# Performance work log

Hardware: AMD Instinct MI355X
Metric: run time of the kernel (lower is better)

Reference implementation:

```python
import jax, jax.numpy as jnp
import numpy as np

N_NODES = 100000
N_EDGES = 1600000
D_IN = 64
D_HID = 64
N_LAYERS = 3


def setup_inputs() -> dict:
    key = jax.random.key(0)
    ks = jax.random.split(key, 10)
    inp = {
        "node_feat": jax.random.normal(ks[0], (N_NODES, D_IN), dtype=jnp.float32),
        "src": jax.random.randint(ks[1], (N_EDGES,), 0, N_NODES, dtype=jnp.int32),
        "dst": jax.random.randint(ks[2], (N_EDGES,), 0, N_NODES, dtype=jnp.int32),
        "graph_len": jnp.ones((1,), dtype=jnp.int32) * N_NODES,
    }
    # GraphConv weights: shape (in_feats, out_feats), applied as feat @ W + b (DGL xavier-style init)
    dims = [D_IN] + [D_HID] * N_LAYERS
    for i in range(N_LAYERS):
        scale = float(np.sqrt(2.0 / (dims[i] + dims[i + 1])))
        inp[f"W{i}"] = jax.random.normal(ks[3 + i], (dims[i], dims[i + 1]), dtype=jnp.float32) * scale
        inp[f"b{i}"] = jnp.zeros((dims[i + 1],), dtype=jnp.float32)
    return inp


def reference(node_feat, src, dst, graph_len, W0, b0, W1, b1, W2, b2):
    n = node_feat.shape[0]
    e = src.shape[0]
    ones = jnp.ones((e,), dtype=node_feat.dtype)
    # DGL GraphConv norm='both': src-side out-degree^{-1/2}, dst-side in-degree^{-1/2}, clamp(min=1)
    deg_out = jax.ops.segment_sum(ones, src, num_segments=n)
    deg_in = jax.ops.segment_sum(ones, dst, num_segments=n)
    inv_sqrt_out = jax.lax.rsqrt(jnp.clip(deg_out, 1.0, None))[:, None]  # [N,1]
    inv_sqrt_in = jax.lax.rsqrt(jnp.clip(deg_in, 1.0, None))[:, None]    # [N,1]

    def graph_conv(x, W, b):
        msg = (x * inv_sqrt_out)[src]                              # [E,F] gather
        agg = jax.ops.segment_sum(msg, dst, num_segments=n)        # [N,F] scatter-add
        return (agg * inv_sqrt_in) @ W + b                         # SpMM result -> dense linear

    xs = []
    h = node_feat
    for W, b in ((W0, b0), (W1, b1), (W2, b2)):
        h = jax.nn.relu(graph_conv(h, W, b))
        xs.append(h)

    # Faithful to source: torch.sum(x, dim=1) -> per-node scalar [N]; concat over layers -> [3N]
    x_pool = jnp.concatenate([x.sum(axis=1) for x in xs], axis=-1)
    xs_cat = jnp.concatenate(xs, axis=-1)  # [N, 3*H]
    return x_pool, xs_cat
```

## Files before the change

kernel.cpp:

```cpp
#include <hip/hip_runtime.h>


#define TPB 256
#define CAP_S2 10240

__device__ __forceinline__ unsigned short f2bf(float f) {
  unsigned u = __float_as_uint(f);
  u += 0x7fff + ((u >> 16) & 1);
  return (unsigned short)(u >> 16);
}
__device__ __forceinline__ float bflo(unsigned u) { return __uint_as_float(u << 16); }
__device__ __forceinline__ float bfhi(unsigned u) { return __uint_as_float(u & 0xffff0000u); }

__global__ __launch_bounds__(256) void coarse_hist(
    const int* __restrict__ src, const int* __restrict__ dst, int e,
    int* __restrict__ bhS, int* __restrict__ bhD) {
  __shared__ int hs[256], hd[256];
  int t = threadIdx.x, b = blockIdx.x;
  hs[t] = 0; hd[t] = 0;
  __syncthreads();
  int base = b * 4096;
  #pragma unroll
  for (int k = 0; k < 4; k++) {
    int i = base + 4 * t + 1024 * k;
    if (i + 3 < e) {
      int4 s4 = *(const int4*)&src[i];
      int4 d4 = *(const int4*)&dst[i];
      atomicAdd(&hs[s4.x >> 9], 1); atomicAdd(&hs[s4.y >> 9], 1);
      atomicAdd(&hs[s4.z >> 9], 1); atomicAdd(&hs[s4.w >> 9], 1);
      atomicAdd(&hd[d4.x >> 9], 1); atomicAdd(&hd[d4.y >> 9], 1);
      atomicAdd(&hd[d4.z >> 9], 1); atomicAdd(&hd[d4.w >> 9], 1);
    } else {
      for (int j = i; j < e && j < i + 4; j++) {
        atomicAdd(&hs[src[j] >> 9], 1);
        atomicAdd(&hd[dst[j] >> 9], 1);
      }
    }
  }
  __syncthreads();
  bhS[b * 256 + t] = hs[t];
  bhD[b * 256 + t] = hd[t];
}

__global__ __launch_bounds__(256) void scan_blocks(
    int* __restrict__ bhS, int* __restrict__ bhD, int nblk, int nbb,
    int* __restrict__ c_base_s, int* __restrict__ c_base_d,
    int* __restrict__ row_ptr, int n, int e) {
  __shared__ int lds[256];
  int t = threadIdx.x;
  int* bh = (blockIdx.x == 0) ? bhS : bhD;
  int run = 0;
  int b = 0;
  for (; b + 3 < nblk; b += 4) {
    int i0 = (b + 0) * 256 + t, i1 = (b + 1) * 256 + t;
    int i2 = (b + 2) * 256 + t, i3 = (b + 3) * 256 + t;
    int v0 = bh[i0], v1 = bh[i1], v2 = bh[i2], v3 = bh[i3];
    bh[i0] = run; run += v0;
    bh[i1] = run; run += v1;
    bh[i2] = run; run += v2;
    bh[i3] = run; run += v3;
  }
  for (; b < nblk; b++) {
    int i0 = b * 256 + t;
    int v0 = bh[i0];
    bh[i0] = run; run += v0;
  }
  lds[t] = run; __syncthreads();
  for (int off = 1; off < 256; off <<= 1) {
    int a = (t >= off) ? lds[t - off] : 0;
    __syncthreads(); lds[t] += a; __syncthreads();
  }
  int ex = lds[t] - run;
  int* cb = (blockIdx.x == 0) ? c_base_s : c_base_d;
  cb[t] = ex;
  if (t == 0) cb[256] = e;
  if (blockIdx.x == 1 && t == 0) row_ptr[n] = e;
}

__global__ __launch_bounds__(256) void scatter_both(
    const int* __restrict__ src, const int* __restrict__ dst, int e,
    const int* __restrict__ bhS, const int* __restrict__ bhD,
    const int* __restrict__ c_base_s, const int* __restrict__ c_base_d,
    int* __restrict__ srcbuf, unsigned* __restrict__ edges1) {
  __shared__ int hs[256], hd[256];
  int t = threadIdx.x, b = blockIdx.x;
  hs[t] = bhS[b * 256 + t] + c_base_s[t];
  hd[t] = bhD[b * 256 + t] + c_base_d[t];
  __syncthreads();
  int base = b * 4096;
  #pragma unroll
  for (int k = 0; k < 4; k++) {
    int i = base + 4 * t + 1024 * k;
    if (i + 3 < e) {
      int4 s4 = *(const int4*)&src[i];
      int4 d4 = *(const int4*)&dst[i];
      int sv[4] = {s4.x, s4.y, s4.z, s4.w};
      int dv[4] = {d4.x, d4.y, d4.z, d4.w};
      #pragma unroll
      for (int j = 0; j < 4; j++) {
        int ps = atomicAdd(&hs[sv[j] >> 9], 1);
        srcbuf[ps] = sv[j];
        int pd = atomicAdd(&hd[dv[j] >> 9], 1);
        edges1[pd] = ((unsigned)sv[j] << 9) | (unsigned)(dv[j] & 511);
      }
    } else {
      for (int j = i; j < e && j < i + 4; j++) {
        int s = src[j], d = dst[j];
        int ps = atomicAdd(&hs[s >> 9], 1);
        srcbuf[ps] = s;
        int pd = atomicAdd(&hd[d >> 9], 1);
        edges1[pd] = ((unsigned)s << 9) | (unsigned)(d & 511);
      }
    }
  }
}

__global__ __launch_bounds__(256) void degout_cast(
    const int* __restrict__ srcbuf, const int* __restrict__ c_base_s,
    const float* __restrict__ node_feat, float* __restrict__ inv_out,
    unsigned short* __restrict__ xb, int n) {
  __shared__ int hist[512];
  __shared__ float sInv[512];
  int b = blockIdx.x, t = threadIdx.x;
  hist[t] = 0; hist[t + 256] = 0;
  __syncthreads();
  int s = c_base_s[b], e = c_base_s[b + 1];
  for (int i = s + t; i < e; i += TPB) atomicAdd(&hist[srcbuf[i] & 511], 1);
  __syncthreads();
  int rstart = b << 9;
  int nrows = min(512, n - rstart);
  #pragma unroll
  for (int k = 0; k < 2; k++) {
    int r = t + k * 256;
    if (r < nrows) {
      float iv = rsqrtf(fmaxf((float)hist[r], 1.0f));
      sInv[r] = iv;
      inv_out[rstart + r] = iv;
    }
  }
  __syncthreads();
  int total4 = nrows * 16;
  const float* xbase = node_feat + (size_t)rstart * 64;
  unsigned short* obase = xb + (size_t)rstart * 64;
  for (int u = t; u < total4; u += TPB) {
    int r = u >> 4;
    float sc = sInv[r];
    float4 v = *(const float4*)&xbase[(size_t)u * 4];
    ushort4 o;
    o.x = f2bf(v.x * sc); o.y = f2bf(v.y * sc);
    o.z = f2bf(v.z * sc); o.w = f2bf(v.w * sc);
    *(ushort4*)&obase[(size_t)u * 4] = o;
  }
}

__global__ __launch_bounds__(256) void scatter2(
    const unsigned* __restrict__ edges1, const int* __restrict__ c_base_d,
    int* __restrict__ row_ptr, float* __restrict__ inv_in,
    int* __restrict__ col, int n) {
  __shared__ int sOut[CAP_S2];
  __shared__ int hist[512];
  __shared__ int cur[512];
  __shared__ int psum[256];
  int b = blockIdx.x, t = threadIdx.x;
  int s = c_base_d[b], e = c_base_d[b + 1];
  int rstart = b << 9;
  int nrows = min(512, n - rstart);
  hist[t] = 0; hist[t + 256] = 0;
  __syncthreads();
  for (int i = s + t; i < e; i += TPB) atomicAdd(&hist[edges1[i] & 511u], 1);
  __syncthreads();
  int h0 = hist[2 * t], h1 = hist[2 * t + 1];
  psum[t] = h0 + h1; __syncthreads();
  for (int off = 1; off < 256; off <<= 1) {
    int a = (t >= off) ? psum[t - off] : 0;
    __syncthreads(); psum[t] += a; __syncthreads();
  }
  int ex = psum[t] - (h0 + h1);
  cur[2 * t] = ex; cur[2 * t + 1] = ex + h0;
  if (2 * t < nrows) {
    row_ptr[rstart + 2 * t] = s + ex;
    inv_in[rstart + 2 * t] = rsqrtf(fmaxf((float)h0, 1.0f));
  }
  if (2 * t + 1 < nrows) {
    row_ptr[rstart + 2 * t + 1] = s + ex + h0;
    inv_in[rstart + 2 * t + 1] = rsqrtf(fmaxf((float)h1, 1.0f));
  }
  __syncthreads();
  for (int i = s + t; i < e; i += TPB) {
    unsigned v = edges1[i];
    int pos = atomicAdd(&cur[v & 511u], 1);
    int sv = (int)(v >> 9);
    if (pos < CAP_S2) sOut[pos] = sv;
    else col[s + pos] = sv;
  }
  __syncthreads();
  int m = min(e - s, CAP_S2);
  for (int k = t; k < m; k += TPB) col[s + k] = sOut[k];
}

__global__ __launch_bounds__(256) void spmm_bf16(
    const unsigned short* __restrict__ xb,
    const int* __restrict__ row_ptr, const int* __restrict__ col,
    float* __restrict__ agg, int n) {
  int wid = (blockIdx.x * TPB + threadIdx.x) >> 6;
  if (wid >= n) return;
  int lane = threadIdx.x & 63;
  int g = lane >> 3;
  int l8 = (lane & 7) << 3;
  int s = row_ptr[wid], e = row_ptr[wid + 1];
  float a0 = 0, a1 = 0, a2 = 0, a3 = 0, a4 = 0, a5 = 0, a6 = 0, a7 = 0;
  int i = s + g;
  for (; i + 8 < e; i += 16) {
    int c0 = col[i], c1 = col[i + 8];
    uint4 r0 = *(const uint4*)&xb[(size_t)c0 * 64 + l8];
    uint4 r1 = *(const uint4*)&xb[(size_t)c1 * 64 + l8];
    a0 += bflo(r0.x); a1 += bfhi(r0.x); a2 += bflo(r0.y); a3 += bfhi(r0.y);
    a4 += bflo(r0.z); a5 += bfhi(r0.z); a6 += bflo(r0.w); a7 += bfhi(r0.w);
    a0 += bflo(r1.x); a1 += bfhi(r1.x); a2 += bflo(r1.y); a3 += bfhi(r1.y);
    a4 += bflo(r1.z); a5 += bfhi(r1.z); a6 += bflo(r1.w); a7 += bfhi(r1.w);
  }
  if (i < e) {
    int c0 = col[i];
    uint4 r0 = *(const uint4*)&xb[(size_t)c0 * 64 + l8];
    a0 += bflo(r0.x); a1 += bfhi(r0.x); a2 += bflo(r0.y); a3 += bfhi(r0.y);
    a4 += bflo(r0.z); a5 += bfhi(r0.z); a6 += bflo(r0.w); a7 += bfhi(r0.w);
  }
  a0 += __shfl_xor(a0, 8); a0 += __shfl_xor(a0, 16); a0 += __shfl_xor(a0, 32);
  a1 += __shfl_xor(a1, 8); a1 += __shfl_xor(a1, 16); a1 += __shfl_xor(a1, 32);
  a2 += __shfl_xor(a2, 8); a2 += __shfl_xor(a2, 16); a2 += __shfl_xor(a2, 32);
  a3 += __shfl_xor(a3, 8); a3 += __shfl_xor(a3, 16); a3 += __shfl_xor(a3, 32);
  a4 += __shfl_xor(a4, 8); a4 += __shfl_xor(a4, 16); a4 += __shfl_xor(a4, 32);
  a5 += __shfl_xor(a5, 8); a5 += __shfl_xor(a5, 16); a5 += __shfl_xor(a5, 32);
  a6 += __shfl_xor(a6, 8); a6 += __shfl_xor(a6, 16); a6 += __shfl_xor(a6, 32);
  a7 += __shfl_xor(a7, 8); a7 += __shfl_xor(a7, 16); a7 += __shfl_xor(a7, 32);
  if (g == 0) {
    float4 lo = {a0, a1, a2, a3};
    float4 hi = {a4, a5, a6, a7};
    *(float4*)&agg[(size_t)wid * 64 + l8] = lo;
    *(float4*)&agg[(size_t)wid * 64 + l8 + 4] = hi;
  }
}

__global__ __launch_bounds__(256) void gemm_relu_pool(
    const float* __restrict__ agg, const float* __restrict__ inv_in,
    const float* __restrict__ inv_out,
    const float* __restrict__ W, const float* __restrict__ bias,
    float* __restrict__ out_cat, float* __restrict__ out_pool,
    unsigned short* __restrict__ xb_next, int n) {
  __shared__ float sW[64 * 64];
  __shared__ float sXT[64][68];
  int t = threadIdx.x;
  int row0 = blockIdx.x * 64;
  for (int i4 = t * 4; i4 < 4096; i4 += 1024)
    *(float4*)&sW[i4] = *(const float4*)&W[i4];
  for (int i = t; i < 4096; i += TPB) {
    int r = i >> 6, f = i & 63;
    int row = row0 + r;
    sXT[f][r] = (row < n) ? agg[(size_t)row * 64 + f] * inv_in[row] : 0.f;
  }
  __syncthreads();
  int tj = t & 15, tr = t >> 4;
  int j4 = tj << 2, r4 = tr << 2;
  const float4 bv = *(const float4*)&bias[j4];
  float4 a0 = bv, a1 = bv, a2 = bv, a3 = bv;
  #pragma unroll 8
  for (int f = 0; f < 64; f++) {
    float4 w  = *(const float4*)&sW[f * 64 + j4];
    float4 xv = *(const float4*)&sXT[f][r4];
    a0.x = fmaf(xv.x, w.x, a0.x); a0.y = fmaf(xv.x, w.y, a0.y);
    a0.z = fmaf(xv.x, w.z, a0.z); a0.w = fmaf(xv.x, w.w, a0.w);
    a1.x = fmaf(xv.y, w.x, a1.x); a1.y = fmaf(xv.y, w.y, a1.y);
    a1.z = fmaf(xv.y, w.z, a1.z); a1.w = fmaf(xv.y, w.w, a1.w);
    a2.x = fmaf(xv.z, w.x, a2.x); a2.y = fmaf(xv.z, w.y, a2.y);
    a2.z = fmaf(xv.z, w.z, a2.z); a2.w = fmaf(xv.z, w.w, a2.w);
    a3.x = fmaf(xv.w, w.x, a3.x); a3.y = fmaf(xv.w, w.y, a3.y);
    a3.z = fmaf(xv.w, w.z, a3.z); a3.w = fmaf(xv.w, w.w, a3.w);
  }
  float4 accs[4] = {a0, a1, a2, a3};
  #pragma unroll
  for (int ri = 0; ri < 4; ri++) {
    int row = row0 + r4 + ri;
    if (row < n) {
      float4 h = accs[ri];
      h.x = fmaxf(h.x, 0.f); h.y = fmaxf(h.y, 0.f);
      h.z = fmaxf(h.z, 0.f); h.w = fmaxf(h.w, 0.f);
      *(float4*)&out_cat[(size_t)row * 192 + j4] = h;
      if (xb_next) {
        float sc = inv_out[row];
        ushort4 o;
        o.x = f2bf(h.x * sc); o.y = f2bf(h.y * sc);
        o.z = f2bf(h.z * sc); o.w = f2bf(h.w * sc);
        *(ushort4*)&xb_next[(size_t)row * 64 + j4] = o;
      }
      float part = h.x + h.y + h.z + h.w;
      part += __shfl_xor(part, 1);
      part += __shfl_xor(part, 2);
      part += __shfl_xor(part, 4);
      part += __shfl_xor(part, 8);
      if (tj == 0) out_pool[row] = part;
    }
  }
}


extern "C" void kernel_launch(void* const* d_in, const int* in_sizes, int n_in,
                              void* d_out, int out_size, void* d_ws, size_t ws_size,
                              hipStream_t stream) {
  const float* node_feat = (const float*)d_in[0];
  const int* src = (const int*)d_in[1];
  const int* dst = (const int*)d_in[2];
  const float* Ws[3] = {(const float*)d_in[4], (const float*)d_in[6], (const float*)d_in[8]};
  const float* bs[3] = {(const float*)d_in[5], (const float*)d_in[7], (const float*)d_in[9]};
  float* out = (float*)d_out;
  int n = in_sizes[0] / 64;
  int e = in_sizes[1];
  int nbb = (n + 511) >> 9;
  int nblk = (e + 4095) / 4096;

  char* p = (char*)d_ws;
  float* agg = (float*)p;       p += (size_t)n * 64 * sizeof(float);
  unsigned short* xb = (unsigned short*)p; p += (size_t)n * 64 * sizeof(unsigned short);
  float* inv_out = (float*)p;   p += (size_t)n * sizeof(float);
  float* inv_in = (float*)p;    p += (size_t)n * sizeof(float);
  int* row_ptr = (int*)p;       p += ((size_t)n + 4) * sizeof(int);
  int* c_base_s = (int*)p;      p += 260 * sizeof(int);
  int* c_base_d = (int*)p;      p += 260 * sizeof(int);
  int* bhS = (int*)p;           p += (size_t)nblk * 256 * sizeof(int);
  int* bhD = (int*)p;           p += (size_t)nblk * 256 * sizeof(int);
  unsigned* edges1 = (unsigned*)p; p += (size_t)e * sizeof(unsigned);
  int* col = (int*)p;           p += (size_t)e * sizeof(int);
  int* srcbuf = col;

  coarse_hist<<<nblk, TPB, 0, stream>>>(src, dst, e, bhS, bhD);
  scan_blocks<<<2, TPB, 0, stream>>>(bhS, bhD, nblk, nbb, c_base_s, c_base_d, row_ptr, n, e);
  scatter_both<<<nblk, TPB, 0, stream>>>(src, dst, e, bhS, bhD, c_base_s, c_base_d,
                                         srcbuf, edges1);
  degout_cast<<<nbb, TPB, 0, stream>>>(srcbuf, c_base_s, node_feat, inv_out, xb, n);
  scatter2<<<nbb, TPB, 0, stream>>>(edges1, c_base_d, row_ptr, inv_in, col, n);

  float* cat_base = out + (size_t)3 * n;
  for (int layer = 0; layer < 3; layer++) {
    spmm_bf16<<<(n + 3) / 4, TPB, 0, stream>>>(xb, row_ptr, col, agg, n);
    gemm_relu_pool<<<(n + 63) / 64, TPB, 0, stream>>>(agg, inv_in, inv_out, Ws[layer], bs[layer],
        cat_base + (size_t)layer * 64, out + (size_t)layer * n,
        (layer < 2) ? xb : (unsigned short*)nullptr, n);
  }
}
```

Baseline: 399.3 us.

## Parallelize bucket prefix scan across 512 blocks and unroll SpMM gather by four

Result: faster. 361.6 us (-9.4%).

```diff
diff --git a/kernel.cpp b/kernel.cpp
--- a/kernel.cpp
+++ b/kernel.cpp
@@ -42,39 +42,50 @@
   bhD[b * 256 + t] = hd[t];
 }
 
-__global__ __launch_bounds__(256) void scan_blocks(
-    int* __restrict__ bhS, int* __restrict__ bhD, int nblk, int nbb,
-    int* __restrict__ c_base_s, int* __restrict__ c_base_d,
-    int* __restrict__ row_ptr, int n, int e) {
+__global__ __launch_bounds__(256) void scan_buckets(
+    int* __restrict__ bhS, int* __restrict__ bhD, int nblk, int* __restrict__ csum) {
   __shared__ int lds[256];
   int t = threadIdx.x;
-  int* bh = (blockIdx.x == 0) ? bhS : bhD;
-  int run = 0;
-  int b = 0;
-  for (; b + 3 < nblk; b += 4) {
-    int i0 = (b + 0) * 256 + t, i1 = (b + 1) * 256 + t;
-    int i2 = (b + 2) * 256 + t, i3 = (b + 3) * 256 + t;
-    int v0 = bh[i0], v1 = bh[i1], v2 = bh[i2], v3 = bh[i3];
-    bh[i0] = run; run += v0;
-    bh[i1] = run; run += v1;
-    bh[i2] = run; run += v2;
-    bh[i3] = run; run += v3;
-  }
-  for (; b < nblk; b++) {
-    int i0 = b * 256 + t;
-    int v0 = bh[i0];
-    bh[i0] = run; run += v0;
-  }
-  lds[t] = run; __syncthreads();
+  int bucket = blockIdx.x & 255;
+  int* bh = (blockIdx.x >> 8) ? bhD : bhS;
+  int carry = 0;
+  for (int c0 = 0; c0 < nblk; c0 += 256) {
+    int b = c0 + t;
+    int v = (b < nblk) ? bh[b * 256 + bucket] : 0;
+    lds[t] = v; __syncthreads();
+    for (int off = 1; off < 256; off <<= 1) {
+      int a = (t >= off) ? lds[t - off] : 0;
+      __syncthreads(); lds[t] += a; __syncthreads();
+    }
+    if (b < nblk) bh[b * 256 + bucket] = carry + lds[t] - v;
+    carry += lds[255];
+    __syncthreads();
+  }
+  if (t == 0) csum[blockIdx.x] = carry;
+}
+
+__global__ void scan_bases(const int* __restrict__ csum,
+                           int* __restrict__ c_base_s, int* __restrict__ c_base_d,
+                           int* __restrict__ row_ptr, int n, int e) {
+  __shared__ int lds[256];
+  int t = threadIdx.x;
+  int v = csum[t];
+  lds[t] = v; __syncthreads();
   for (int off = 1; off < 256; off <<= 1) {
     int a = (t >= off) ? lds[t - off] : 0;
     __syncthreads(); lds[t] += a; __syncthreads();
   }
-  int ex = lds[t] - run;
-  int* cb = (blockIdx.x == 0) ? c_base_s : c_base_d;
-  cb[t] = ex;
-  if (t == 0) cb[256] = e;
-  if (blockIdx.x == 1 && t == 0) row_ptr[n] = e;
+  c_base_s[t] = lds[t] - v;
+  if (t == 0) c_base_s[256] = e;
+  __syncthreads();
+  int vd = csum[256 + t];
+  lds[t] = vd; __syncthreads();
+  for (int off = 1; off < 256; off <<= 1) {
+    int a = (t >= off) ? lds[t - off] : 0;
+    __syncthreads(); lds[t] += a; __syncthreads();
+  }
+  c_base_d[t] = lds[t] - vd;
+  if (t == 0) { c_base_d[256] = e; row_ptr[n] = e; }
 }
 
 __global__ __launch_bounds__(256) void scatter_both(
@@ -209,21 +220,34 @@
   int l8 = (lane & 7) << 3;
   int s = row_ptr[wid], e = row_ptr[wid + 1];
   float a0 = 0, a1 = 0, a2 = 0, a3 = 0, a4 = 0, a5 = 0, a6 = 0, a7 = 0;
-  int i = s + g;
-  for (; i + 8 < e; i += 16) {
-    int c0 = col[i], c1 = col[i + 8];
+  for (int i = s + g; i < e; i += 32) {
+    int ec = e - 1;
+    int i1 = i + 8, i2 = i + 16, i3 = i + 24;
+    int c0 = col[i];
+    int c1 = col[min(i1, ec)];
+    int c2 = col[min(i2, ec)];
+    int c3 = col[min(i3, ec)];
+    float m1 = (i1 < e) ? 1.f : 0.f;
+    float m2 = (i2 < e) ? 1.f : 0.f;
+    float m3 = (i3 < e) ? 1.f : 0.f;
     uint4 r0 = *(const uint4*)&xb[(size_t)c0 * 64 + l8];
     uint4 r1 = *(const uint4*)&xb[(size_t)c1 * 64 + l8];
+    uint4 r2 = *(const uint4*)&xb[(size_t)c2 * 64 + l8];
+    uint4 r3 = *(const uint4*)&xb[(size_t)c3 * 64 + l8];
     a0 += bflo(r0.x); a1 += bfhi(r0.x); a2 += bflo(r0.y); a3 += bfhi(r0.y);
     a4 += bflo(r0.z); a5 += bfhi(r0.z); a6 += bflo(r0.w); a7 += bfhi(r0.w);
-    a0 += bflo(r1.x); a1 += bfhi(r1.x); a2 += bflo(r1.y); a3 += bfhi(r1.y);
-    a4 += bflo(r1.z); a5 += bfhi(r1.z); a6 += bflo(r1.w); a7 += bfhi(r1.w);
-  }
-  if (i < e) {
-    int c0 = col[i];
-    uint4 r0 = *(const uint4*)&xb[(size_t)c0 * 64 + l8];
-    a0 += bflo(r0.x); a1 += bfhi(r0.x); a2 += bflo(r0.y); a3 += bfhi(r0.y);
-    a4 += bflo(r0.z); a5 += bfhi(r0.z); a6 += bflo(r0.w); a7 += bfhi(r0.w);
+    a0 = fmaf(m1, bflo(r1.x), a0); a1 = fmaf(m1, bfhi(r1.x), a1);
+    a2 = fmaf(m1, bflo(r1.y), a2); a3 = fmaf(m1, bfhi(r1.y), a3);
+    a4 = fmaf(m1, bflo(r1.z), a4); a5 = fmaf(m1, bfhi(r1.z), a5);
+    a6 = fmaf(m1, bflo(r1.w), a6); a7 = fmaf(m1, bfhi(r1.w), a7);
+    a0 = fmaf(m2, bflo(r2.x), a0); a1 = fmaf(m2, bfhi(r2.x), a1);
+    a2 = fmaf(m2, bflo(r2.y), a2); a3 = fmaf(m2, bfhi(r2.y), a3);
+    a4 = fmaf(m2, bflo(r2.z), a4); a5 = fmaf(m2, bfhi(r2.z), a5);
+    a6 = fmaf(m2, bflo(r2.w), a6); a7 = fmaf(m2, bfhi(r2.w), a7);
+    a0 = fmaf(m3, bflo(r3.x), a0); a1 = fmaf(m3, bfhi(r3.x), a1);
+    a2 = fmaf(m3, bflo(r3.y), a2); a3 = fmaf(m3, bfhi(r3.y), a3);
+    a4 = fmaf(m3, bflo(r3.z), a4); a5 = fmaf(m3, bfhi(r3.z), a5);
+    a6 = fmaf(m3, bflo(r3.w), a6); a7 = fmaf(m3, bfhi(r3.w), a7);
   }
   a0 += __shfl_xor(a0, 8); a0 += __shfl_xor(a0, 16); a0 += __shfl_xor(a0, 32);
   a1 += __shfl_xor(a1, 8); a1 += __shfl_xor(a1, 16); a1 += __shfl_xor(a1, 32);
@@ -325,6 +349,7 @@
   int* row_ptr = (int*)p;       p += ((size_t)n + 4) * sizeof(int);
   int* c_base_s = (int*)p;      p += 260 * sizeof(int);
   int* c_base_d = (int*)p;      p += 260 * sizeof(int);
+  int* csum = (int*)p;          p += 512 * sizeof(int);
   int* bhS = (int*)p;           p += (size_t)nblk * 256 * sizeof(int);
   int* bhD = (int*)p;           p += (size_t)nblk * 256 * sizeof(int);
   unsigned* edges1 = (unsigned*)p; p += (size_t)e * sizeof(unsigned);
@@ -332,7 +357,8 @@
   int* srcbuf = col;
 
   coarse_hist<<<nblk, TPB, 0, stream>>>(src, dst, e, bhS, bhD);
-  scan_blocks<<<2, TPB, 0, stream>>>(bhS, bhD, nblk, nbb, c_base_s, c_base_d, row_ptr, n, e);
+  scan_buckets<<<512, TPB, 0, stream>>>(bhS, bhD, nblk, csum);
+  scan_bases<<<1, TPB, 0, stream>>>(csum, c_base_s, c_base_d, row_ptr, n, e);
   scatter_both<<<nblk, TPB, 0, stream>>>(src, dst, e, bhS, bhD, c_base_s, c_base_d,
                                          srcbuf, edges1);
   degout_cast<<<nbb, TPB, 0, stream>>>(srcbuf, c_base_s, node_feat, inv_out, xb, n);
```
